# Performance work log

Measured on AMD Instinct MI355X. Metric: run time of the kernel, lower is better.

Reference implementation:

```python
import jax, jax.numpy as jnp
import numpy as np

DIN = 1024
DOUT = 1024
NUM_HEAD = 16
HEAD_DIM = DIN // NUM_HEAD  # 64
SEQ = 2048
BS = 4


def setup_inputs() -> dict:
    key = jax.random.key(0)
    ks = jax.random.split(key, 9)
    s_in = 1.0 / np.sqrt(DIN)
    s_out = 1.0 / np.sqrt(DOUT)
    return {
        "x": jax.random.normal(ks[0], (BS, SEQ, DIN), dtype=jnp.float32),
        "Wq": jax.random.normal(ks[1], (DIN, DOUT), dtype=jnp.float32) * s_in,
        "bq": jax.random.normal(ks[2], (DOUT,), dtype=jnp.float32) * s_in,
        "Wk": jax.random.normal(ks[3], (DIN, DOUT), dtype=jnp.float32) * s_in,
        "bk": jax.random.normal(ks[4], (DOUT,), dtype=jnp.float32) * s_in,
        "Wv": jax.random.normal(ks[5], (DIN, DOUT), dtype=jnp.float32) * s_in,
        "bv": jax.random.normal(ks[6], (DOUT,), dtype=jnp.float32) * s_in,
        "Wo": jax.random.normal(ks[7], (DOUT, DOUT), dtype=jnp.float32) * s_out,
        "bo": jax.random.normal(ks[8], (DOUT,), dtype=jnp.float32) * s_out,
    }


def reference(x, Wq, bq, Wk, bk, Wv, bv, Wo, bo):
    bs, n, _ = x.shape
    # projections -> [bs, n, H, hd] -> [bs, H, n, hd]
    def split_heads(t):
        return t.reshape(bs, n, NUM_HEAD, HEAD_DIM).transpose(0, 2, 1, 3)

    q = split_heads(x @ Wq + bq)
    k = split_heads(x @ Wk + bk)
    v = split_heads(x @ Wv + bv)

    # full [bs, H, n, n] scores, causal mask, scaled softmax
    scores = jnp.einsum("bhqd,bhkd->bhqk", q, k)
    causal = jnp.tril(jnp.ones((n, n), dtype=bool))
    scores = jnp.where(causal, scores, -jnp.inf)
    att = jax.nn.softmax(scores / np.sqrt(HEAD_DIM), axis=-1)

    ctx = jnp.einsum("bhqk,bhkd->bhqd", att, v)
    ctx = ctx.transpose(0, 2, 1, 3).reshape(bs, n, DOUT)
    return ctx @ Wo + bo
```

## Files before the change

kernel.cpp:

```cpp
#include <hip/hip_runtime.h>
#include <hip/hip_bf16.h>
#include <stdint.h>

#define DIN   1024
#define DOUT  1024
#define NHEAD 16
#define HDIM  64
#define SEQL  2048
#define BSZ   4
#define MTOT  (BSZ*SEQL)
#define KDIM  1024

typedef __bf16 bf16x8 __attribute__((ext_vector_type(8)));
typedef float  f32x4  __attribute__((ext_vector_type(4)));

__device__ __forceinline__ f32x4 mfma16(bf16x8 a, bf16x8 b, f32x4 c) {
    return __builtin_amdgcn_mfma_f32_16x16x32_bf16(a, b, c, 0, 0, 0);
}

__device__ __forceinline__ void gl_lds16(const void* gsrc, void* ldst) {
    __builtin_amdgcn_global_load_lds(
        (const __attribute__((address_space(1))) uint32_t*)gsrc,
        (__attribute__((address_space(3))) uint32_t*)ldst, 16, 0, 0);
}

#if __has_builtin(__builtin_amdgcn_exp2f)
__device__ __forceinline__ float fexp2(float x) { return __builtin_amdgcn_exp2f(x); }
#else
__device__ __forceinline__ float fexp2(float x) { return exp2f(x); }
#endif

__device__ __forceinline__ unsigned int cvtpk(float lo, float hi) {
    unsigned int r;
    asm("v_cvt_pk_bf16_f32 %0, %1, %2" : "=v"(r) : "v"(lo), "v"(hi));
    return r;
}

__device__ __forceinline__ unsigned short f2bf(float f) {
    union { __hip_bfloat16 h; unsigned short u; } cv;
    cv.h = __float2bfloat16(f);
    return cv.u;
}

__global__ void cvt_bf16(const float4* __restrict__ in, ushort4* __restrict__ out, int n4) {
    int idx = blockIdx.x * blockDim.x + threadIdx.x;
    int stride = gridDim.x * blockDim.x;
    for (int i = idx; i < n4; i += stride) {
        float4 v = in[i];
        ushort4 o;
        o.x = f2bf(v.x); o.y = f2bf(v.y); o.z = f2bf(v.z); o.w = f2bf(v.w);
        out[i] = o;
    }
}

__global__ void transpose_cvt3(const float* __restrict__ W0, const float* __restrict__ W1,
                               const float* __restrict__ W2, __hip_bfloat16* __restrict__ Wt3) {
    __shared__ __hip_bfloat16 t[32][33];
    const int tx = threadIdx.x, ty = threadIdx.y;
    const int bx = blockIdx.x, by = blockIdx.y, z = blockIdx.z;
    const float* W = (z == 0) ? W0 : (z == 1) ? W1 : W2;
    __hip_bfloat16* Wt = Wt3 + (size_t)z * DOUT * DIN;
#pragma unroll
    for (int r = 0; r < 4; ++r)
        t[ty + 8*r][tx] = __float2bfloat16(W[(size_t)(by*32 + ty + 8*r) * DOUT + bx*32 + tx]);
    __syncthreads();
#pragma unroll
    for (int r = 0; r < 4; ++r)
        Wt[(size_t)(bx*32 + ty + 8*r) * DIN + by*32 + tx] = t[tx][ty + 8*r];
}

__global__ void transpose_cvt(const float* __restrict__ W, __hip_bfloat16* __restrict__ Wt) {
    __shared__ __hip_bfloat16 t[32][33];
    const int tx = threadIdx.x, ty = threadIdx.y;
    const int bx = blockIdx.x, by = blockIdx.y;
#pragma unroll
    for (int r = 0; r < 4; ++r)
        t[ty + 8*r][tx] = __float2bfloat16(W[(size_t)(by*32 + ty + 8*r) * DOUT + bx*32 + tx]);
    __syncthreads();
#pragma unroll
    for (int r = 0; r < 4; ++r)
        Wt[(size_t)(bx*32 + ty + 8*r) * DIN + by*32 + tx] = t[tx][ty + 8*r];
}

template <int EPI>
__global__ __launch_bounds__(256)
void gemm_mfma(const __hip_bfloat16* __restrict__ A,
               const __hip_bfloat16* __restrict__ Bt,
               const float* __restrict__ b0, const float* __restrict__ b1,
               void* __restrict__ o0, void* __restrict__ o1,
               float scale)
{
    __shared__ alignas(16) __hip_bfloat16 As[2][4][128][8];
    __shared__ alignas(16) __hip_bfloat16 Bs[2][4][128][8];

    const int tid  = threadIdx.x;
    const int w    = tid >> 6;
    const int lane = tid & 63;
    const int g    = lane >> 4;
    const int r    = lane & 15;
    const int wr   = w >> 1, wc = w & 1;

    const int row0 = blockIdx.y * 128;
    const int col0 = blockIdx.x * 128;

    f32x4 acc[4][4];
#pragma unroll
    for (int m = 0; m < 4; ++m)
#pragma unroll
        for (int n = 0; n < 4; ++n) acc[m][n] = (f32x4)0.0f;

    auto stage = [&](int buf, int kt) {
        const __hip_bfloat16* ga = A  + (size_t)(row0 + lane) * KDIM + kt*32 + 8*w;
        const __hip_bfloat16* gb = Bt + (size_t)(col0 + lane) * KDIM + kt*32 + 8*w;
        gl_lds16(ga,            &As[buf][w][0][0]);
        gl_lds16(ga + 64*KDIM,  &As[buf][w][64][0]);
        gl_lds16(gb,            &Bs[buf][w][0][0]);
        gl_lds16(gb + 64*KDIM,  &Bs[buf][w][64][0]);
    };

    stage(0, 0);
    __syncthreads();

    const int NKT = KDIM / 32;
    for (int kt = 0; kt < NKT; ++kt) {
        const int cur = kt & 1;
        if (kt + 1 < NKT) stage(cur ^ 1, kt + 1);

        bf16x8 af[4], bfr[4];
#pragma unroll
        for (int m = 0; m < 4; ++m)
            af[m] = *reinterpret_cast<const bf16x8*>(&As[cur][g][64*wr + 16*m + r][0]);
#pragma unroll
        for (int n = 0; n < 4; ++n)
            bfr[n] = *reinterpret_cast<const bf16x8*>(&Bs[cur][g][64*wc + 16*n + r][0]);

#pragma unroll
        for (int m = 0; m < 4; ++m)
#pragma unroll
            for (int n = 0; n < 4; ++n) {
                if (EPI == 1) acc[m][n] = mfma16(af[m], bfr[n], acc[m][n]);
                else          acc[m][n] = mfma16(bfr[n], af[m], acc[m][n]);
            }

        __syncthreads();
    }

    if (EPI == 0) {
        const int slab = col0 >> 10;
        const float* bp = (slab == 0) ? b0 : b1;
        __hip_bfloat16* op = (__hip_bfloat16*)((slab == 0) ? o0 : o1);
        const float sc = (slab == 0) ? scale : 1.0f;
#pragma unroll
        for (int m = 0; m < 4; ++m) {
            const int rowg = row0 + 64*wr + 16*m + r;
            const int bb = rowg >> 11, sq = rowg & (SEQL-1);
#pragma unroll
            for (int n = 0; n < 4; ++n) {
                const int c2 = (col0 & 1023) + 64*wc + 16*n + 4*g;
                const int hh = c2 >> 6, dd = c2 & (HDIM-1);
                const float4 bv4 = *reinterpret_cast<const float4*>(&bp[c2]);
                ushort4 ov;
                ov.x = f2bf((acc[m][n][0] + bv4.x) * sc);
                ov.y = f2bf((acc[m][n][1] + bv4.y) * sc);
                ov.z = f2bf((acc[m][n][2] + bv4.z) * sc);
                ov.w = f2bf((acc[m][n][3] + bv4.w) * sc);
                *reinterpret_cast<ushort4*>(
                    &op[(((size_t)(bb*NHEAD + hh) * SEQL + sq) << 6) + dd]) = ov;
            }
        }
    } else if (EPI == 1) {
#pragma unroll
        for (int n = 0; n < 4; ++n) {
            const int colg = col0 + 64*wc + 16*n + r;
            const int hh = colg >> 6, dd = colg & (HDIM-1);
            const float bv_ = b0[colg];
#pragma unroll
            for (int m = 0; m < 4; ++m) {
                const int rowg0 = row0 + 64*wr + 16*m + 4*g;
                const int bb = rowg0 >> 11, sq0 = rowg0 & (SEQL-1);
                ushort4 ov;
                ov.x = f2bf(acc[m][n][0] + bv_);
                ov.y = f2bf(acc[m][n][1] + bv_);
                ov.z = f2bf(acc[m][n][2] + bv_);
                ov.w = f2bf(acc[m][n][3] + bv_);
                *reinterpret_cast<ushort4*>(
                    &((__hip_bfloat16*)o0)[((size_t)(bb*NHEAD + hh) * HDIM + dd) * SEQL + sq0]) = ov;
            }
        }
    } else {
#pragma unroll
        for (int m = 0; m < 4; ++m) {
            const int rowg = row0 + 64*wr + 16*m + r;
#pragma unroll
            for (int n = 0; n < 4; ++n) {
                const int colg0 = col0 + 64*wc + 16*n + 4*g;
                const float4 bv4 = *reinterpret_cast<const float4*>(&b0[colg0]);
                float4 ov;
                ov.x = acc[m][n][0] + bv4.x;
                ov.y = acc[m][n][1] + bv4.y;
                ov.z = acc[m][n][2] + bv4.z;
                ov.w = acc[m][n][3] + bv4.w;
                *reinterpret_cast<float4*>(&((float*)o0)[(size_t)rowg * DOUT + colg0]) = ov;
            }
        }
    }
}

__global__ __launch_bounds__(256)
void attn_fwd(const __hip_bfloat16* __restrict__ Q,
              const __hip_bfloat16* __restrict__ K,
              const __hip_bfloat16* __restrict__ Vt,
              __hip_bfloat16* __restrict__ ctx)
{
    __shared__ alignas(16) __hip_bfloat16 Ps[4][2][16][64];
    __shared__ alignas(16) f32x4 Om[2][64][8];
    __shared__ float Ml[2][64][5];

    const int tid  = threadIdx.x;
    const int w    = tid >> 6;
    const int lane = tid & 63;
    const int g    = lane >> 4;
    const int r    = lane & 15;
    const int swz  = (r & 7) << 3;
    const int pp   = w >> 1;
    const int half = w & 1;

    const int bh = blockIdx.x;
    const int b  = bh >> 4, h = bh & 15;

    const __hip_bfloat16* Qh = Q  + (size_t)bh * SEQL * HDIM;
    const __hip_bfloat16* Kh = K  + (size_t)bh * SEQL * HDIM;
    const __hip_bfloat16* Vh = Vt + (size_t)bh * HDIM * SEQL;

    const int sp = blockIdx.y * 2 + pp;

#pragma unroll 1
    for (int ti = 0; ti < 2; ++ti) {
        const int strip = ti ? (63 - sp) : sp;
        const int qb = strip * 32;

        bf16x8 qf[2][2];
#pragma unroll
        for (int m = 0; m < 2; ++m)
#pragma unroll
            for (int hh = 0; hh < 2; ++hh)
                qf[m][hh] = *reinterpret_cast<const bf16x8*>(
                    Qh + (size_t)(qb + 16*m + r) * HDIM + 32*hh + 8*g);

        f32x4 o[2][4];
        float mrow[2], lrow[2];
#pragma unroll
        for (int m = 0; m < 2; ++m) {
#pragma unroll
            for (int n = 0; n < 4; ++n) o[m][n] = (f32x4)0.0f;
            mrow[m] = -1e30f; lrow[m] = 0.0f;
        }

        const int nst = ((qb + 31) >> 6) + 1;
        const int ns2 = (nst + 1) >> 1;
        const int k0  = half ? ns2 : 0;
        const int k1  = half ? nst : ns2;

        const __hip_bfloat16* kp01 = Kh + (size_t)(k0*64 + r) * HDIM + 8*g;
        const __hip_bfloat16* kp23 = kp01 + 32*HDIM;
        const __hip_bfloat16* vp0  = Vh + (size_t)r * SEQL + (size_t)k0*64 + 8*g;
        const __hip_bfloat16* vp1  = vp0 + (size_t)16*SEQL;
        const __hip_bfloat16* vp2  = vp0 + (size_t)32*SEQL;
        const __hip_bfloat16* vp3  = vp0 + (size_t)48*SEQL;

#pragma unroll 1
        for (int kt = k0; kt < k1; ++kt) {
            const int key0 = kt * 64;

            bf16x8 kf[4][2], vf[4][2];
#pragma unroll
            for (int hh = 0; hh < 2; ++hh) {
                kf[0][hh] = *reinterpret_cast<const bf16x8*>(kp01 + hh*32);
                kf[1][hh] = *reinterpret_cast<const bf16x8*>(kp01 + 16*HDIM + hh*32);
                kf[2][hh] = *reinterpret_cast<const bf16x8*>(kp23 + hh*32);
                kf[3][hh] = *reinterpret_cast<const bf16x8*>(kp23 + 16*HDIM + hh*32);
                vf[0][hh] = *reinterpret_cast<const bf16x8*>(vp0 + hh*32);
                vf[1][hh] = *reinterpret_cast<const bf16x8*>(vp1 + hh*32);
                vf[2][hh] = *reinterpret_cast<const bf16x8*>(vp2 + hh*32);
                vf[3][hh] = *reinterpret_cast<const bf16x8*>(vp3 + hh*32);
            }
            kp01 += 64*HDIM; kp23 += 64*HDIM;
            vp0 += 64; vp1 += 64; vp2 += 64; vp3 += 64;

            f32x4 s[2][4];
            __builtin_amdgcn_s_setprio(1);
#pragma unroll
            for (int m = 0; m < 2; ++m)
#pragma unroll
                for (int c = 0; c < 4; ++c) {
                    f32x4 t = (f32x4)0.0f;
                    t = mfma16(kf[c][0], qf[m][0], t);
                    t = mfma16(kf[c][1], qf[m][1], t);
                    s[m][c] = t;
                }
            __builtin_amdgcn_s_setprio(0);

            if (kt == nst - 1) {
#pragma unroll
                for (int m = 0; m < 2; ++m) {
                    const int qrow = qb + 16*m + r;
#pragma unroll
                    for (int c = 0; c < 4; ++c) {
                        const int kb = key0 + 16*c + 4*g;
#pragma unroll
                        for (int j = 0; j < 4; ++j)
                            if (kb + j > qrow) s[m][c][j] = -1e30f;
                    }
                }
            }

#pragma unroll
            for (int m = 0; m < 2; ++m) {
                float t0 = fmaxf(fmaxf(s[m][0][0], s[m][0][1]), fmaxf(s[m][0][2], s[m][0][3]));
                float t1 = fmaxf(fmaxf(s[m][1][0], s[m][1][1]), fmaxf(s[m][1][2], s[m][1][3]));
                float t2 = fmaxf(fmaxf(s[m][2][0], s[m][2][1]), fmaxf(s[m][2][2], s[m][2][3]));
                float t3 = fmaxf(fmaxf(s[m][3][0], s[m][3][1]), fmaxf(s[m][3][2], s[m][3][3]));
                float pml = fmaxf(fmaxf(t0, t1), fmaxf(t2, t3));

                if (__any(pml > mrow[m] + 11.0f)) {
                    float pm = fmaxf(pml, __shfl_xor(pml, 16));
                    pm = fmaxf(pm, __shfl_xor(pm, 32));
                    const float mnew = fmaxf(mrow[m], pm);
                    const float fac  = fexp2(mrow[m] - mnew);
                    mrow[m] = mnew;
                    lrow[m] *= fac;
#pragma unroll
                    for (int n = 0; n < 4; ++n) o[m][n] *= fac;
                }

                float p[4][4];
#pragma unroll
                for (int c = 0; c < 4; ++c)
#pragma unroll
                    for (int j = 0; j < 4; ++j)
                        p[c][j] = fexp2(s[m][c][j] - mrow[m]);

                float u0 = (p[0][0] + p[0][1]) + (p[0][2] + p[0][3]);
                float u1 = (p[1][0] + p[1][1]) + (p[1][2] + p[1][3]);
                float u2 = (p[2][0] + p[2][1]) + (p[2][2] + p[2][3]);
                float u3 = (p[3][0] + p[3][1]) + (p[3][2] + p[3][3]);
                lrow[m] += (u0 + u1) + (u2 + u3);

#pragma unroll
                for (int c = 0; c < 4; ++c) {
                    uint2 pk;
                    pk.x = cvtpk(p[c][0], p[c][1]);
                    pk.y = cvtpk(p[c][2], p[c][3]);
                    *reinterpret_cast<uint2*>(&Ps[w][m][r][(16*c + 4*g) ^ swz]) = pk;
                }
            }

            bf16x8 pf[2][2];
#pragma unroll
            for (int m = 0; m < 2; ++m)
#pragma unroll
                for (int hh = 0; hh < 2; ++hh)
                    pf[m][hh] = *reinterpret_cast<const bf16x8*>(
                        &Ps[w][m][r][(32*hh + 8*g) ^ swz]);

            __builtin_amdgcn_s_setprio(1);
#pragma unroll
            for (int n = 0; n < 4; ++n)
#pragma unroll
                for (int m = 0; m < 2; ++m) {
                    o[m][n] = mfma16(vf[n][0], pf[m][0], o[m][n]);
                    o[m][n] = mfma16(vf[n][1], pf[m][1], o[m][n]);
                }
            __builtin_amdgcn_s_setprio(0);
        }

#pragma unroll
        for (int m = 0; m < 2; ++m) {
            lrow[m] += __shfl_xor(lrow[m], 16);
            lrow[m] += __shfl_xor(lrow[m], 32);
        }

        if (half) {
#pragma unroll
            for (int m = 0; m < 2; ++m)
#pragma unroll
                for (int n = 0; n < 4; ++n)
                    Om[pp][lane][(m*4 + n) ^ (lane & 7)] = o[m][n];
            Ml[pp][lane][0] = mrow[0];
            Ml[pp][lane][1] = mrow[1];
            Ml[pp][lane][2] = lrow[0];
            Ml[pp][lane][3] = lrow[1];
        }
        __syncthreads();
        if (!half) {
#pragma unroll
            for (int m = 0; m < 2; ++m) {
                const float m1 = Ml[pp][lane][m];
                const float l1 = Ml[pp][lane][2 + m];
                const float M  = fmaxf(mrow[m], m1);
                const float f0 = fexp2(mrow[m] - M);
                const float f1 = fexp2(m1 - M);
                const float L  = lrow[m] * f0 + l1 * f1;
                const float inv = 1.0f / L;
                const size_t rowbase = (size_t)(b*SEQL + qb + 16*m + r) * DOUT + h*HDIM;
#pragma unroll
                for (int n = 0; n < 4; ++n) {
                    const f32x4 o1 = Om[pp][lane][(m*4 + n) ^ (lane & 7)];
                    uint2 ov;
                    ov.x = cvtpk((o[m][n][0]*f0 + o1[0]*f1) * inv,
                                 (o[m][n][1]*f0 + o1[1]*f1) * inv);
                    ov.y = cvtpk((o[m][n][2]*f0 + o1[2]*f1) * inv,
                                 (o[m][n][3]*f0 + o1[3]*f1) * inv);
                    *reinterpret_cast<uint2*>(&ctx[rowbase + 16*n + 4*g]) = ov;
                }
            }
        }
        __syncthreads();
    }
}

extern "C" void kernel_launch(void* const* d_in, const int* in_sizes, int n_in,
                              void* d_out, int out_size, void* d_ws, size_t ws_size,
                              hipStream_t stream) {
    const float* x  = (const float*)d_in[0];
    const float* Wq = (const float*)d_in[1];
    const float* bq = (const float*)d_in[2];
    const float* Wk = (const float*)d_in[3];
    const float* bk = (const float*)d_in[4];
    const float* Wv = (const float*)d_in[5];
    const float* bv = (const float*)d_in[6];
    const float* Wo = (const float*)d_in[7];
    const float* bo = (const float*)d_in[8];
    float* out = (float*)d_out;
    (void)in_sizes; (void)n_in; (void)out_size; (void)ws_size;

    char* ws = (char*)d_ws;
    __hip_bfloat16* xb  = (__hip_bfloat16*)ws;
    __hip_bfloat16* Wt3 = (__hip_bfloat16*)(ws + (16u << 20));
    __hip_bfloat16* Wot = (__hip_bfloat16*)(ws + (22u << 20));
    __hip_bfloat16* Qb  = (__hip_bfloat16*)(ws + (24u << 20));
    __hip_bfloat16* Kb  = Qb + (size_t)MTOT * DOUT;
    __hip_bfloat16* Vtb = Kb + (size_t)MTOT * DOUT;
    __hip_bfloat16* ctx = xb;

    cvt_bf16<<<2048, 256, 0, stream>>>((const float4*)x, (ushort4*)xb, MTOT * DIN / 4);

    dim3 tb(32, 8);
    transpose_cvt3<<<dim3(32, 32, 3), tb, 0, stream>>>(Wq, Wk, Wv, Wt3);
    transpose_cvt <<<dim3(32, 32),    tb, 0, stream>>>(Wo, Wot);

    dim3 gqk(2*DOUT / 128, MTOT / 128);
    gemm_mfma<0><<<gqk, 256, 0, stream>>>(xb, Wt3, bq, bk, Qb, Kb,
                                          0.125f * 1.44269504088896f);
    dim3 gv(DOUT / 128, MTOT / 128);
    gemm_mfma<1><<<gv, 256, 0, stream>>>(xb, Wt3 + (size_t)2*DOUT*DIN, bv, nullptr,
                                         Vtb, nullptr, 1.0f);

    dim3 ag(BSZ * NHEAD, 16);
    attn_fwd<<<ag, 256, 0, stream>>>(Qb, Kb, Vtb, ctx);

    gemm_mfma<2><<<gv, 256, 0, stream>>>(ctx, Wot, bo, nullptr,
                                         out, nullptr, 1.0f);
}
```

Measured before the change: 305.2 us.

## Widen attention query tile per wave from 32 to 64 rows

Each wave now processes 64 query rows (four 16-row MFMA tiles) per strip instead of 32, so every K/V fragment loaded from global memory is reused across twice as many queries. The grid's y dimension is halved and the softmax/PV work is restructured into a per-m-tile loop that reuses a single P scratch buffer. This trades halved K/V load traffic for doubled accumulator registers (possibly lower occupancy), fewer blocks (64x8=512), and coarser causal granularity, since the full 64-key diagonal tile is now computed for every 64-row strip.

```diff
diff --git a/kernel.cpp b/kernel.cpp
--- a/kernel.cpp
+++ b/kernel.cpp
@@ -212,9 +212,9 @@
               const __hip_bfloat16* __restrict__ Vt,
               __hip_bfloat16* __restrict__ ctx)
 {
-    __shared__ alignas(16) __hip_bfloat16 Ps[4][2][16][64];
-    __shared__ alignas(16) f32x4 Om[2][64][8];
-    __shared__ float Ml[2][64][5];
+    __shared__ alignas(16) __hip_bfloat16 Ps[4][16][64];
+    __shared__ alignas(16) f32x4 Om[2][64][16];
+    __shared__ float Ml[2][64][9];
 
     const int tid  = threadIdx.x;
     const int w    = tid >> 6;
@@ -236,27 +236,27 @@
 
 #pragma unroll 1
     for (int ti = 0; ti < 2; ++ti) {
-        const int strip = ti ? (63 - sp) : sp;
-        const int qb = strip * 32;
-
-        bf16x8 qf[2][2];
-#pragma unroll
-        for (int m = 0; m < 2; ++m)
+        const int strip = ti ? (31 - sp) : sp;
+        const int qb = strip * 64;
+
+        bf16x8 qf[4][2];
+#pragma unroll
+        for (int m = 0; m < 4; ++m)
 #pragma unroll
             for (int hh = 0; hh < 2; ++hh)
                 qf[m][hh] = *reinterpret_cast<const bf16x8*>(
                     Qh + (size_t)(qb + 16*m + r) * HDIM + 32*hh + 8*g);
 
-        f32x4 o[2][4];
-        float mrow[2], lrow[2];
-#pragma unroll
-        for (int m = 0; m < 2; ++m) {
+        f32x4 o[4][4];
+        float mrow[4], lrow[4];
+#pragma unroll
+        for (int m = 0; m < 4; ++m) {
 #pragma unroll
             for (int n = 0; n < 4; ++n) o[m][n] = (f32x4)0.0f;
             mrow[m] = -1e30f; lrow[m] = 0.0f;
         }
 
-        const int nst = ((qb + 31) >> 6) + 1;
+        const int nst = strip + 1;
         const int ns2 = (nst + 1) >> 1;
         const int k0  = half ? ns2 : 0;
         const int k1  = half ? nst : ns2;
@@ -287,39 +287,36 @@
             kp01 += 64*HDIM; kp23 += 64*HDIM;
             vp0 += 64; vp1 += 64; vp2 += 64; vp3 += 64;
 
-            f32x4 s[2][4];
-            __builtin_amdgcn_s_setprio(1);
-#pragma unroll
-            for (int m = 0; m < 2; ++m)
+            const bool lastkt = (kt == nst - 1);
+
+#pragma unroll
+            for (int m = 0; m < 4; ++m) {
+                f32x4 s[4];
+                __builtin_amdgcn_s_setprio(1);
 #pragma unroll
                 for (int c = 0; c < 4; ++c) {
                     f32x4 t = (f32x4)0.0f;
                     t = mfma16(kf[c][0], qf[m][0], t);
                     t = mfma16(kf[c][1], qf[m][1], t);
-                    s[m][c] = t;
-                }
-            __builtin_amdgcn_s_setprio(0);
-
-            if (kt == nst - 1) {
-#pragma unroll
-                for (int m = 0; m < 2; ++m) {
-                    const int qrow = qb + 16*m + r;
+                    s[c] = t;
+                }
+                __builtin_amdgcn_s_setprio(0);
+
+                const int qrow = qb + 16*m + r;
+                if (lastkt) {
 #pragma unroll
                     for (int c = 0; c < 4; ++c) {
                         const int kb = key0 + 16*c + 4*g;
 #pragma unroll
                         for (int j = 0; j < 4; ++j)
-                            if (kb + j > qrow) s[m][c][j] = -1e30f;
+                            if (kb + j > qrow) s[c][j] = -1e30f;
                     }
                 }
-            }
-
-#pragma unroll
-            for (int m = 0; m < 2; ++m) {
-                float t0 = fmaxf(fmaxf(s[m][0][0], s[m][0][1]), fmaxf(s[m][0][2], s[m][0][3]));
-                float t1 = fmaxf(fmaxf(s[m][1][0], s[m][1][1]), fmaxf(s[m][1][2], s[m][1][3]));
-                float t2 = fmaxf(fmaxf(s[m][2][0], s[m][2][1]), fmaxf(s[m][2][2], s[m][2][3]));
-                float t3 = fmaxf(fmaxf(s[m][3][0], s[m][3][1]), fmaxf(s[m][3][2], s[m][3][3]));
+
+                float t0 = fmaxf(fmaxf(s[0][0], s[0][1]), fmaxf(s[0][2], s[0][3]));
+                float t1 = fmaxf(fmaxf(s[1][0], s[1][1]), fmaxf(s[1][2], s[1][3]));
+                float t2 = fmaxf(fmaxf(s[2][0], s[2][1]), fmaxf(s[2][2], s[2][3]));
+                float t3 = fmaxf(fmaxf(s[3][0], s[3][1]), fmaxf(s[3][2], s[3][3]));
                 float pml = fmaxf(fmaxf(t0, t1), fmaxf(t2, t3));
 
                 if (__any(pml > mrow[m] + 11.0f)) {
@@ -338,7 +335,7 @@
                 for (int c = 0; c < 4; ++c)
 #pragma unroll
                     for (int j = 0; j < 4; ++j)
-                        p[c][j] = fexp2(s[m][c][j] - mrow[m]);
+                        p[c][j] = fexp2(s[c][j] - mrow[m]);
 
                 float u0 = (p[0][0] + p[0][1]) + (p[0][2] + p[0][3]);
                 float u1 = (p[1][0] + p[1][1]) + (p[1][2] + p[1][3]);
@@ -351,52 +348,47 @@
                     uint2 pk;
                     pk.x = cvtpk(p[c][0], p[c][1]);
                     pk.y = cvtpk(p[c][2], p[c][3]);
-                    *reinterpret_cast<uint2*>(&Ps[w][m][r][(16*c + 4*g) ^ swz]) = pk;
-                }
-            }
-
-            bf16x8 pf[2][2];
-#pragma unroll
-            for (int m = 0; m < 2; ++m)
+                    *reinterpret_cast<uint2*>(&Ps[w][r][(16*c + 4*g) ^ swz]) = pk;
+                }
+
+                bf16x8 pf[2];
 #pragma unroll
                 for (int hh = 0; hh < 2; ++hh)
-                    pf[m][hh] = *reinterpret_cast<const bf16x8*>(
-                        &Ps[w][m][r][(32*hh + 8*g) ^ swz]);
-
-            __builtin_amdgcn_s_setprio(1);
-#pragma unroll
-            for (int n = 0; n < 4; ++n)
-#pragma unroll
-                for (int m = 0; m < 2; ++m) {
-                    o[m][n] = mfma16(vf[n][0], pf[m][0], o[m][n]);
-                    o[m][n] = mfma16(vf[n][1], pf[m][1], o[m][n]);
-                }
-            __builtin_amdgcn_s_setprio(0);
-        }
-
-#pragma unroll
-        for (int m = 0; m < 2; ++m) {
+                    pf[hh] = *reinterpret_cast<const bf16x8*>(
+                        &Ps[w][r][(32*hh + 8*g) ^ swz]);
+
+                __builtin_amdgcn_s_setprio(1);
+#pragma unroll
+                for (int n = 0; n < 4; ++n) {
+                    o[m][n] = mfma16(vf[n][0], pf[0], o[m][n]);
+                    o[m][n] = mfma16(vf[n][1], pf[1], o[m][n]);
+                }
+                __builtin_amdgcn_s_setprio(0);
+            }
+        }
+
+#pragma unroll
+        for (int m = 0; m < 4; ++m) {
             lrow[m] += __shfl_xor(lrow[m], 16);
             lrow[m] += __shfl_xor(lrow[m], 32);
         }
 
         if (half) {
 #pragma unroll
-            for (int m = 0; m < 2; ++m)
+            for (int m = 0; m < 4; ++m) {
 #pragma unroll
                 for (int n = 0; n < 4; ++n)
                     Om[pp][lane][(m*4 + n) ^ (lane & 7)] = o[m][n];
-            Ml[pp][lane][0] = mrow[0];
-            Ml[pp][lane][1] = mrow[1];
-            Ml[pp][lane][2] = lrow[0];
-            Ml[pp][lane][3] = lrow[1];
+                Ml[pp][lane][m]     = mrow[m];
+                Ml[pp][lane][4 + m] = lrow[m];
+            }
         }
         __syncthreads();
         if (!half) {
 #pragma unroll
-            for (int m = 0; m < 2; ++m) {
+            for (int m = 0; m < 4; ++m) {
                 const float m1 = Ml[pp][lane][m];
-                const float l1 = Ml[pp][lane][2 + m];
+                const float l1 = Ml[pp][lane][4 + m];
                 const float M  = fmaxf(mrow[m], m1);
                 const float f0 = fexp2(mrow[m] - M);
                 const float f1 = fexp2(m1 - M);
@@ -456,7 +448,7 @@
     gemm_mfma<1><<<gv, 256, 0, stream>>>(xb, Wt3 + (size_t)2*DOUT*DIN, bv, nullptr,
                                          Vtb, nullptr, 1.0f);
 
-    dim3 ag(BSZ * NHEAD, 16);
+    dim3 ag(BSZ * NHEAD, 8);
     attn_fwd<<<ag, 256, 0, stream>>>(Qb, Kb, Vtb, ctx);
 
     gemm_mfma<2><<<gv, 256, 0, stream>>>(ctx, Wot, bo, nullptr,
```

Measured after the change: 269.1 us. -11.8%, faster.
